# Optimization experiments

Measured on AMD Instinct MI355X. Metric: run time of the kernel, lower is better.

## Reference

```python
import jax, jax.numpy as jnp
import numpy as np

EPS = 1e-5

def layer_norm(x, g, b):
    mu = jnp.mean(x, axis=-1, keepdims=True)
    var = jnp.mean(jnp.square(x - mu), axis=-1, keepdims=True)
    return (x - mu) * jax.lax.rsqrt(var + EPS) * g + b

def setup_inputs() -> dict:
    B, T, C, H = 8, 1024, 1024, 16
    hs = C // H
    key = jax.random.key(0)
    ks = jax.random.split(key, 12)
    s = 0.02
    return {
        "x": jax.random.normal(ks[0], (B, T, C), dtype=jnp.float32),
        # per-head projections, stacked: [H, C, hs]
        "wq": jax.random.normal(ks[1], (H, C, hs), dtype=jnp.float32) * s,
        "wk": jax.random.normal(ks[2], (H, C, hs), dtype=jnp.float32) * s,
        "wv": jax.random.normal(ks[3], (H, C, hs), dtype=jnp.float32) * s,
        "w_proj": jax.random.normal(ks[4], (C, C), dtype=jnp.float32) * s,
        "b_proj": jnp.zeros((C,), dtype=jnp.float32),
        "ln1_g": jnp.ones((C,), dtype=jnp.float32),
        "ln1_b": jnp.zeros((C,), dtype=jnp.float32),
        "ln2_g": jnp.ones((C,), dtype=jnp.float32),
        "ln2_b": jnp.zeros((C,), dtype=jnp.float32),
        "w1": jax.random.normal(ks[5], (C, 4 * C), dtype=jnp.float32) * s,
        "b1": jnp.zeros((4 * C,), dtype=jnp.float32),
        "w2": jax.random.normal(ks[6], (4 * C, C), dtype=jnp.float32) * s,
        "b2": jnp.zeros((C,), dtype=jnp.float32),
    }

def reference(x, wq, wk, wv, w_proj, b_proj, ln1_g, ln1_b, ln2_g, ln2_b, w1, b1, w2, b2):
    B, T, C = x.shape
    # --- self-attention (pre-norm) ---
    h = layer_norm(x, ln1_g, ln1_b)                      # [B,T,C]
    q = jnp.einsum('btc,hcd->bhtd', h, wq)               # [B,H,T,hs]
    k = jnp.einsum('btc,hcd->bhtd', h, wk)
    v = jnp.einsum('btc,hcd->bhtd', h, wv)
    # NOTE: original scales by C**-0.5 with C = n_embed (not head_size)
    scores = jnp.einsum('bhtd,bhsd->bhts', q, k) * (C ** -0.5)
    causal = jnp.tril(jnp.ones((T, T), dtype=bool))
    scores = jnp.where(causal, scores, -jnp.inf)
    att = jax.nn.softmax(scores, axis=-1)                # dropout is identity (eval)
    out = jnp.einsum('bhts,bhsd->bhtd', att, v)          # [B,H,T,hs]
    out = out.transpose(0, 2, 1, 3).reshape(B, T, C)     # concat heads
    x = x + out @ w_proj + b_proj
    # --- feed-forward (pre-norm) ---
    h2 = layer_norm(x, ln2_g, ln2_b)
    x = x + jax.nn.relu(h2 @ w1 + b1) @ w2 + b2
    return x
```

## Files before the change

kernel.cpp:

```cpp
#include <hip/hip_runtime.h>
#include <cstdint>

typedef __attribute__((ext_vector_type(8))) __bf16 bf16x8;
typedef __attribute__((ext_vector_type(4))) float f32x4;

__device__ __forceinline__ unsigned short f2bf(float f) {
  union { float f; unsigned int u; } v; v.f = f;
  unsigned int u = v.u;
  return (unsigned short)((u + 0x7FFFu + ((u >> 16) & 1u)) >> 16);
}

__device__ __forceinline__ void load_lds16(const unsigned short* g, unsigned short* l) {
  __builtin_amdgcn_global_load_lds(
      (const __attribute__((address_space(1))) unsigned int*)g,
      (__attribute__((address_space(3))) unsigned int*)l, 16, 0, 0);
}

__global__ void prep_kernel(const float* __restrict__ wq, const float* __restrict__ wk,
                            const float* __restrict__ wv, const float* __restrict__ w_proj,
                            const float* __restrict__ w1, const float* __restrict__ w2,
                            const float* __restrict__ x, const float* __restrict__ ln1_g,
                            const float* __restrict__ ln1_b,
                            unsigned short* __restrict__ qkvt, unsigned short* __restrict__ projt,
                            unsigned short* __restrict__ w1t, unsigned short* __restrict__ w2t,
                            unsigned short* __restrict__ h1) {
  __shared__ float tile[32][33];
  __shared__ float a1[4], a2[4];
  const int id = blockIdx.x;
  const int tid = threadIdx.x;

  if (id >= 12288) {
    const int row = id - 12288;
    const int wave = tid >> 6, lane = tid & 63;
    const float4 xv = *(const float4*)&x[(long)row * 1024 + tid * 4];
    float s1 = xv.x + xv.y + xv.z + xv.w;
    float s2 = xv.x * xv.x + xv.y * xv.y + xv.z * xv.z + xv.w * xv.w;
#pragma unroll
    for (int m = 1; m < 64; m <<= 1) { s1 += __shfl_xor(s1, m); s2 += __shfl_xor(s2, m); }
    if (lane == 0) { a1[wave] = s1; a2[wave] = s2; }
    __syncthreads();
    s1 = a1[0] + a1[1] + a1[2] + a1[3];
    s2 = a2[0] + a2[1] + a2[2] + a2[3];
    const float mu = s1 * (1.f / 1024.f);
    const float var = s2 * (1.f / 1024.f) - mu * mu;
    const float rs = rsqrtf(var + 1e-5f);
    const float4 gv = *(const float4*)&ln1_g[tid * 4];
    const float4 bv = *(const float4*)&ln1_b[tid * 4];
    ushort4 o;
    o.x = f2bf((xv.x - mu) * rs * gv.x + bv.x);
    o.y = f2bf((xv.y - mu) * rs * gv.y + bv.y);
    o.z = f2bf((xv.z - mu) * rs * gv.z + bv.z);
    o.w = f2bf((xv.w - mu) * rs * gv.w + bv.w);
    *(ushort4*)&h1[(long)row * 1024 + tid * 4] = o;
    return;
  }

  const float* src;
  unsigned short* dst;
  int K, N, nt, kt;
  if (id < 3072) {
    const int which = id >> 10, rem = id & 1023;
    const int slice = rem >> 6, t = rem & 63;
    src = (which == 0 ? wq : which == 1 ? wk : wv) + (long)slice * 65536;
    dst = qkvt + (long)which * 1048576 + (long)slice * 65536;
    K = 1024; N = 64;
    nt = (t & 1) * 32; kt = (t >> 1) * 32;
  } else if (id < 4096) {
    const int t = id - 3072;
    src = w_proj; dst = projt; K = 1024; N = 1024;
    nt = (t & 31) * 32; kt = (t >> 5) * 32;
  } else if (id < 8192) {
    const int t = id - 4096;
    src = w1; dst = w1t; K = 1024; N = 4096;
    nt = (t & 127) * 32; kt = (t >> 7) * 32;
  } else {
    const int t = id - 8192;
    src = w2; dst = w2t; K = 4096; N = 1024;
    nt = (t & 31) * 32; kt = (t >> 5) * 32;
  }
  const int tx = tid & 31, ty = tid >> 5;
#pragma unroll
  for (int i = 0; i < 4; i++)
    tile[ty + 8 * i][tx] = src[(long)(kt + ty + 8 * i) * N + nt + tx];
  __syncthreads();
#pragma unroll
  for (int i = 0; i < 4; i++)
    dst[(long)(nt + ty + 8 * i) * K + kt + tx] = f2bf(tile[tx][ty + 8 * i]);
}

__global__ __launch_bounds__(256, 4) void ln_kernel(const float* __restrict__ x,
                                                    const float* __restrict__ g,
                                                    const float* __restrict__ b,
                                                    unsigned short* __restrict__ out) {
  const int row = blockIdx.x, tid = threadIdx.x;
  const int wave = tid >> 6, lane = tid & 63;
  const float4 xv = *(const float4*)&x[(long)row * 1024 + tid * 4];
  float s1 = xv.x + xv.y + xv.z + xv.w;
  float s2 = xv.x * xv.x + xv.y * xv.y + xv.z * xv.z + xv.w * xv.w;
#pragma unroll
  for (int m = 1; m < 64; m <<= 1) { s1 += __shfl_xor(s1, m); s2 += __shfl_xor(s2, m); }
  __shared__ float a1[4], a2[4];
  if (lane == 0) { a1[wave] = s1; a2[wave] = s2; }
  __syncthreads();
  s1 = a1[0] + a1[1] + a1[2] + a1[3];
  s2 = a2[0] + a2[1] + a2[2] + a2[3];
  const float mu = s1 * (1.f / 1024.f);
  const float var = s2 * (1.f / 1024.f) - mu * mu;
  const float rs = rsqrtf(var + 1e-5f);
  const float4 gv = *(const float4*)&g[tid * 4];
  const float4 bv = *(const float4*)&b[tid * 4];
  ushort4 o;
  o.x = f2bf((xv.x - mu) * rs * gv.x + bv.x);
  o.y = f2bf((xv.y - mu) * rs * gv.y + bv.y);
  o.z = f2bf((xv.z - mu) * rs * gv.z + bv.z);
  o.w = f2bf((xv.w - mu) * rs * gv.w + bv.w);
  *(ushort4*)&out[(long)row * 1024 + tid * 4] = o;
}

#define EPI_QKV 0
#define EPI_F32 1
#define EPI_RELU 2

template <int EPI>
__global__ __launch_bounds__(256, 3) void gemm_bt(
    const unsigned short* __restrict__ A, const unsigned short* __restrict__ Bt,
    int M, int N, int K,
    const float* __restrict__ bias, const float* __restrict__ resid,
    float* __restrict__ outF, unsigned short* __restrict__ outB,
    unsigned short* __restrict__ qb, unsigned short* __restrict__ kb,
    unsigned short* __restrict__ vTb) {
  __shared__ __attribute__((aligned(16))) unsigned short Alds[128 * 64];
  __shared__ __attribute__((aligned(16))) unsigned short Blds[128 * 64];
  const int tid = threadIdx.x;
  const int wave = tid >> 6, lane = tid & 63;
  const int quad = lane >> 4, l15 = lane & 15;
  const long tM = (long)blockIdx.x * 128;
  const long tN = (long)blockIdx.y * 128;
  const int wm = (wave >> 1) * 64, wn = (wave & 1) * 64;

  const unsigned short* aP[4];
  const unsigned short* bP[4];
  unsigned short* lA[4];
  unsigned short* lB[4];
#pragma unroll
  for (int qq = 0; qq < 4; qq++) {
    int p = (qq * 4 + wave) * 64 + lane;
    int m = p >> 3;
    int kc = (p & 7) ^ (m & 7);
    aP[qq] = A + (tM + m) * K + kc * 8;
    bP[qq] = Bt + (tN + m) * K + kc * 8;
    lA[qq] = Alds + (qq * 4 + wave) * 512;
    lB[qq] = Blds + (qq * 4 + wave) * 512;
  }

  f32x4 acc[4][4];
#pragma unroll
  for (int i = 0; i < 4; i++)
#pragma unroll
    for (int j = 0; j < 4; j++) acc[i][j] = (f32x4){0.f, 0.f, 0.f, 0.f};

  for (int k0 = 0; k0 < K; k0 += 64) {
    __syncthreads();
#pragma unroll
    for (int qq = 0; qq < 4; qq++) {
      load_lds16(aP[qq], lA[qq]);
      load_lds16(bP[qq], lB[qq]);
      aP[qq] += 64;
      bP[qq] += 64;
    }
    __syncthreads();
#pragma unroll
    for (int ks = 0; ks < 2; ks++) {
      bf16x8 af[4], bfr[4];
#pragma unroll
      for (int mt = 0; mt < 4; mt++) {
        int ml = wm + mt * 16 + l15;
        int pc = (ks * 4 + quad) ^ (ml & 7);
        af[mt] = *(const bf16x8*)&Alds[(ml * 8 + pc) * 8];
      }
#pragma unroll
      for (int nt = 0; nt < 4; nt++) {
        int nl = wn + nt * 16 + l15;
        int pc = (ks * 4 + quad) ^ (nl & 7);
        bfr[nt] = *(const bf16x8*)&Blds[(nl * 8 + pc) * 8];
      }
#pragma unroll
      for (int mt = 0; mt < 4; mt++)
#pragma unroll
        for (int nt = 0; nt < 4; nt++)
          acc[mt][nt] = __builtin_amdgcn_mfma_f32_16x16x32_bf16(af[mt], bfr[nt], acc[mt][nt], 0, 0, 0);
    }
  }

#pragma unroll
  for (int mt = 0; mt < 4; mt++) {
#pragma unroll
    for (int nt = 0; nt < 4; nt++) {
      const long col = tN + wn + nt * 16 + l15;
      const long row0 = tM + wm + mt * 16 + quad * 4;
      if (EPI == EPI_F32) {
        const float bv = bias[col];
#pragma unroll
        for (int r = 0; r < 4; r++) {
          long idx = (row0 + r) * N + col;
          outF[idx] = acc[mt][nt][r] + bv + resid[idx];
        }
      } else if (EPI == EPI_RELU) {
        const float bv = bias[col];
#pragma unroll
        for (int r = 0; r < 4; r++) {
          float v = acc[mt][nt][r] + bv;
          outB[(row0 + r) * N + col] = f2bf(v > 0.f ? v : 0.f);
        }
      } else {
        const int which = (int)(col >> 10);
        const int hh = (int)((col >> 6) & 15);
        const int dd = (int)(col & 63);
        const int b = (int)(row0 >> 10), t0 = (int)(row0 & 1023);
        if (which == 2) {
          ushort4 pk;
          pk.x = f2bf(acc[mt][nt][0]);
          pk.y = f2bf(acc[mt][nt][1]);
          pk.z = f2bf(acc[mt][nt][2]);
          pk.w = f2bf(acc[mt][nt][3]);
          *(ushort4*)&vTb[(long)(b * 16 + hh) * 65536 + dd * 1024 + t0] = pk;
        } else {
          unsigned short* dst = (which == 0 ? qb : kb);
#pragma unroll
          for (int r = 0; r < 4; r++)
            dst[((b * 16 + hh) * 1024 + t0 + r) * 64 + dd] = f2bf(acc[mt][nt][r]);
        }
      }
    }
  }
}

__global__ __launch_bounds__(256, 2) void attn_kernel(const unsigned short* __restrict__ qb,
                                                      const unsigned short* __restrict__ kb,
                                                      const unsigned short* __restrict__ vTb,
                                                      unsigned short* __restrict__ out) {
  __shared__ __attribute__((aligned(16))) unsigned short Klds[2][64 * 64];
  __shared__ __attribute__((aligned(16))) unsigned short Vlds[2][64 * 64];
  __shared__ __attribute__((aligned(16))) unsigned short Plds[4 * 16 * 68];
  const int bh = blockIdx.x;
  const int j = blockIdx.y;
  const int tid = threadIdx.x;
  const int wave = tid >> 6, lane = tid & 63;
  const int quad = lane >> 4, l15 = lane & 15;

  const unsigned short* qp = qb + (long)bh * 65536;
  const unsigned short* kp = kb + (long)bh * 65536;
  const unsigned short* vp = vTb + (long)bh * 65536;
  const int b = bh >> 4, h = bh & 15;

  unsigned short* Pl = Plds + wave * (16 * 68);
  const float cscale = 0.045084220f;

  for (int ph = 0; ph < 2; ph++) {
    const int qt2 = ph ? 7 - j : j;

    bf16x8 qf[2][2];
#pragma unroll
    for (int g = 0; g < 2; g++) {
      const int qrow = qt2 * 128 + (wave * 2 + g) * 16 + l15;
      qf[g][0] = *(const bf16x8*)&qp[qrow * 64 + quad * 8];
      qf[g][1] = *(const bf16x8*)&qp[qrow * 64 + 32 + quad * 8];
    }

    f32x4 O[2][4];
    float l_r[2][4];
#pragma unroll
    for (int g = 0; g < 2; g++) {
#pragma unroll
      for (int nt = 0; nt < 4; nt++) O[g][nt] = (f32x4){0.f, 0.f, 0.f, 0.f};
#pragma unroll
      for (int r = 0; r < 4; r++) l_r[g][r] = 0.f;
    }

    const int nstage = qt2 + 1;
    for (int st = 0; st < nstage; st++) {
      __syncthreads();
#pragma unroll
      for (int c = 0; c < 4; c++) {
        const int pb = c * 256 + wave * 64;
        const int p = pb + lane;
        const int sub = p >> 9;
        const int q_ = p & 511;
        const int m = q_ >> 3;
        const int kc = (q_ & 7) ^ (m & 7);
        const int kt = st * 2 + sub;
        load_lds16(kp + (kt * 64 + m) * 64 + kc * 8, (unsigned short*)Klds + pb * 8);
        load_lds16(vp + m * 1024 + kt * 64 + kc * 8, (unsigned short*)Vlds + pb * 8);
      }
      __syncthreads();

#pragma unroll
      for (int sub = 0; sub < 2; sub++) {
        const int kt = st * 2 + sub;
        const unsigned short* Ksub = (const unsigned short*)Klds + sub * 4096;
        const unsigned short* Vsub = (const unsigned short*)Vlds + sub * 4096;

#pragma unroll
        for (int g = 0; g < 2; g++) {
          const int rowbase = qt2 * 128 + (wave * 2 + g) * 16;
          if (kt * 64 >= rowbase + 16) continue;

          f32x4 S[4];
#pragma unroll
          for (int nt = 0; nt < 4; nt++) {
            const int row = nt * 16 + l15;
            const int pc0 = quad ^ (row & 7);
            const int pc1 = (quad + 4) ^ (row & 7);
            bf16x8 kf0 = *(const bf16x8*)&Ksub[(row * 8 + pc0) * 8];
            bf16x8 kf1 = *(const bf16x8*)&Ksub[(row * 8 + pc1) * 8];
            f32x4 s = (f32x4){0.f, 0.f, 0.f, 0.f};
            s = __builtin_amdgcn_mfma_f32_16x16x32_bf16(qf[g][0], kf0, s, 0, 0, 0);
            s = __builtin_amdgcn_mfma_f32_16x16x32_bf16(qf[g][1], kf1, s, 0, 0, 0);
            S[nt] = s;
          }

          const bool diag = (kt * 64 + 63 > rowbase);
          const int tb = rowbase + quad * 4;
#pragma unroll
          for (int nt = 0; nt < 4; nt++) {
            const int sg = kt * 64 + nt * 16 + l15;
#pragma unroll
            for (int r = 0; r < 4; r++) {
              float pv = exp2f(S[nt][r] * cscale);
              if (diag && sg > tb + r) pv = 0.f;
              l_r[g][r] += pv;
              Pl[(quad * 4 + r) * 68 + nt * 16 + l15] = f2bf(pv);
            }
          }
          __threadfence_block();

#pragma unroll
          for (int ks2 = 0; ks2 < 2; ks2++) {
            bf16x8 pa = *(const bf16x8*)&Pl[l15 * 68 + ks2 * 32 + quad * 8];
#pragma unroll
            for (int nt = 0; nt < 4; nt++) {
              const int d = nt * 16 + l15;
              const int pc = (ks2 * 4 + quad) ^ (d & 7);
              bf16x8 vf = *(const bf16x8*)&Vsub[(d * 8 + pc) * 8];
              O[g][nt] = __builtin_amdgcn_mfma_f32_16x16x32_bf16(pa, vf, O[g][nt], 0, 0, 0);
            }
          }
          __threadfence_block();
        }
      }
    }

#pragma unroll
    for (int g = 0; g < 2; g++) {
#pragma unroll
      for (int r = 0; r < 4; r++) {
        float lv = l_r[g][r];
        lv += __shfl_xor(lv, 1);
        lv += __shfl_xor(lv, 2);
        lv += __shfl_xor(lv, 4);
        lv += __shfl_xor(lv, 8);
        lv = __builtin_amdgcn_rcpf(lv);
        const int t = qt2 * 128 + (wave * 2 + g) * 16 + quad * 4 + r;
#pragma unroll
        for (int nt = 0; nt < 4; nt++)
          out[(long)(b * 1024 + t) * 1024 + h * 64 + nt * 16 + l15] = f2bf(O[g][nt][r] * lv);
      }
    }
  }
}

extern "C" void kernel_launch(void* const* d_in, const int* in_sizes, int n_in,
                              void* d_out, int out_size, void* d_ws, size_t ws_size,
                              hipStream_t stream) {
  const float* x = (const float*)d_in[0];
  const float* wq = (const float*)d_in[1];
  const float* wk = (const float*)d_in[2];
  const float* wv = (const float*)d_in[3];
  const float* w_proj = (const float*)d_in[4];
  const float* b_proj = (const float*)d_in[5];
  const float* ln1_g = (const float*)d_in[6];
  const float* ln1_b = (const float*)d_in[7];
  const float* ln2_g = (const float*)d_in[8];
  const float* ln2_b = (const float*)d_in[9];
  const float* w1 = (const float*)d_in[10];
  const float* b1 = (const float*)d_in[11];
  const float* w2 = (const float*)d_in[12];
  const float* b2 = (const float*)d_in[13];
  float* out = (float*)d_out;

  char* w = (char*)d_ws;
  unsigned short* h1 = (unsigned short*)w;      w += (size_t)8192 * 1024 * 2;
  unsigned short* wqkvt = (unsigned short*)w;   w += (size_t)3072 * 1024 * 2;
  unsigned short* wprojt = (unsigned short*)w;  w += (size_t)1024 * 1024 * 2;
  unsigned short* w1t = (unsigned short*)w;     w += (size_t)4096 * 1024 * 2;
  unsigned short* w2t = (unsigned short*)w;     w += (size_t)4096 * 1024 * 2;
  unsigned short* qbuf = (unsigned short*)w;    w += (size_t)128 * 1024 * 64 * 2;
  unsigned short* kbuf = (unsigned short*)w;    w += (size_t)128 * 1024 * 64 * 2;
  unsigned short* vTbuf = (unsigned short*)w;   w += (size_t)128 * 1024 * 64 * 2;
  unsigned short* act = (unsigned short*)w;     w += (size_t)8192 * 4096 * 2;
  unsigned short* attnO = h1;
  unsigned short* h2 = qbuf;

  prep_kernel<<<12288 + 8192, 256, 0, stream>>>(wq, wk, wv, w_proj, w1, w2,
                                                x, ln1_g, ln1_b,
                                                wqkvt, wprojt, w1t, w2t, h1);

  gemm_bt<EPI_QKV><<<dim3(64, 24), 256, 0, stream>>>(h1, wqkvt, 8192, 3072, 1024,
                                                     nullptr, nullptr, nullptr, nullptr,
                                                     qbuf, kbuf, vTbuf);

  attn_kernel<<<dim3(128, 4), 256, 0, stream>>>(qbuf, kbuf, vTbuf, attnO);

  gemm_bt<EPI_F32><<<dim3(64, 8), 256, 0, stream>>>(attnO, wprojt, 8192, 1024, 1024,
                                                    b_proj, x, out, nullptr,
                                                    nullptr, nullptr, nullptr);

  ln_kernel<<<8192, 256, 0, stream>>>(out, ln2_g, ln2_b, h2);

  gemm_bt<EPI_RELU><<<dim3(64, 32), 256, 0, stream>>>(h2, w1t, 8192, 4096, 1024,
                                                      b1, nullptr, nullptr, act,
                                                      nullptr, nullptr, nullptr);

  gemm_bt<EPI_F32><<<dim3(64, 8), 256, 0, stream>>>(act, w2t, 8192, 1024, 4096,
                                                    b2, out, out, nullptr,
                                                    nullptr, nullptr, nullptr);
}
```

Measured before the change: 438.4 us.

## Move proj/FFN weight transposes into the QKV GEMM launch as extra blocks

Splits the prep kernel so it only converts the QKV weights and runs layernorm 1. The projection and FFN weight transpose-to-bf16 work is appended as trailing blocks of a dedicated QKV GEMM kernel. The aim is to overlap the memory-bound weight conversion with the compute-bound QKV GEMM and shorten the critical path of the prep stage. In exchange, the GEMM kernel carries extra shared memory for the transpose tile and has heterogeneous blocks, which could affect occupancy or scheduling.

Result: no change. 440.2 us (+0.4%).

```diff
diff --git a/kernel.cpp b/kernel.cpp
--- a/kernel.cpp
+++ b/kernel.cpp
@@ -16,21 +16,18 @@
       (__attribute__((address_space(3))) unsigned int*)l, 16, 0, 0);
 }
 
-__global__ void prep_kernel(const float* __restrict__ wq, const float* __restrict__ wk,
-                            const float* __restrict__ wv, const float* __restrict__ w_proj,
-                            const float* __restrict__ w1, const float* __restrict__ w2,
-                            const float* __restrict__ x, const float* __restrict__ ln1_g,
-                            const float* __restrict__ ln1_b,
-                            unsigned short* __restrict__ qkvt, unsigned short* __restrict__ projt,
-                            unsigned short* __restrict__ w1t, unsigned short* __restrict__ w2t,
-                            unsigned short* __restrict__ h1) {
+__global__ void prep1_kernel(const float* __restrict__ wq, const float* __restrict__ wk,
+                             const float* __restrict__ wv,
+                             const float* __restrict__ x, const float* __restrict__ ln1_g,
+                             const float* __restrict__ ln1_b,
+                             unsigned short* __restrict__ qkvt, unsigned short* __restrict__ h1) {
   __shared__ float tile[32][33];
   __shared__ float a1[4], a2[4];
   const int id = blockIdx.x;
   const int tid = threadIdx.x;
 
-  if (id >= 12288) {
-    const int row = id - 12288;
+  if (id >= 3072) {
+    const int row = id - 3072;
     const int wave = tid >> 6, lane = tid & 63;
     const float4 xv = *(const float4*)&x[(long)row * 1024 + tid * 4];
     float s1 = xv.x + xv.y + xv.z + xv.w;
@@ -55,37 +52,19 @@
     return;
   }
 
-  const float* src;
-  unsigned short* dst;
-  int K, N, nt, kt;
-  if (id < 3072) {
-    const int which = id >> 10, rem = id & 1023;
-    const int slice = rem >> 6, t = rem & 63;
-    src = (which == 0 ? wq : which == 1 ? wk : wv) + (long)slice * 65536;
-    dst = qkvt + (long)which * 1048576 + (long)slice * 65536;
-    K = 1024; N = 64;
-    nt = (t & 1) * 32; kt = (t >> 1) * 32;
-  } else if (id < 4096) {
-    const int t = id - 3072;
-    src = w_proj; dst = projt; K = 1024; N = 1024;
-    nt = (t & 31) * 32; kt = (t >> 5) * 32;
-  } else if (id < 8192) {
-    const int t = id - 4096;
-    src = w1; dst = w1t; K = 1024; N = 4096;
-    nt = (t & 127) * 32; kt = (t >> 7) * 32;
-  } else {
-    const int t = id - 8192;
-    src = w2; dst = w2t; K = 4096; N = 1024;
-    nt = (t & 31) * 32; kt = (t >> 5) * 32;
-  }
+  const int which = id >> 10, rem = id & 1023;
+  const int slice = rem >> 6, t = rem & 63;
+  const float* src = (which == 0 ? wq : which == 1 ? wk : wv) + (long)slice * 65536;
+  unsigned short* dst = qkvt + (long)which * 1048576 + (long)slice * 65536;
+  const int nt = (t & 1) * 32, kt = (t >> 1) * 32;
   const int tx = tid & 31, ty = tid >> 5;
 #pragma unroll
   for (int i = 0; i < 4; i++)
-    tile[ty + 8 * i][tx] = src[(long)(kt + ty + 8 * i) * N + nt + tx];
+    tile[ty + 8 * i][tx] = src[(long)(kt + ty + 8 * i) * 64 + nt + tx];
   __syncthreads();
 #pragma unroll
   for (int i = 0; i < 4; i++)
-    dst[(long)(nt + ty + 8 * i) * K + kt + tx] = f2bf(tile[tx][ty + 8 * i]);
+    dst[(long)(nt + ty + 8 * i) * 1024 + kt + tx] = f2bf(tile[tx][ty + 8 * i]);
 }
 
 __global__ __launch_bounds__(256, 4) void ln_kernel(const float* __restrict__ x,
@@ -117,7 +96,6 @@
   *(ushort4*)&out[(long)row * 1024 + tid * 4] = o;
 }
 
-#define EPI_QKV 0
 #define EPI_F32 1
 #define EPI_RELU 2
 
@@ -126,9 +104,7 @@
     const unsigned short* __restrict__ A, const unsigned short* __restrict__ Bt,
     int M, int N, int K,
     const float* __restrict__ bias, const float* __restrict__ resid,
-    float* __restrict__ outF, unsigned short* __restrict__ outB,
-    unsigned short* __restrict__ qb, unsigned short* __restrict__ kb,
-    unsigned short* __restrict__ vTb) {
+    float* __restrict__ outF, unsigned short* __restrict__ outB) {
   __shared__ __attribute__((aligned(16))) unsigned short Alds[128 * 64];
   __shared__ __attribute__((aligned(16))) unsigned short Blds[128 * 64];
   const int tid = threadIdx.x;
@@ -198,38 +174,149 @@
     for (int nt = 0; nt < 4; nt++) {
       const long col = tN + wn + nt * 16 + l15;
       const long row0 = tM + wm + mt * 16 + quad * 4;
+      const float bv = bias[col];
       if (EPI == EPI_F32) {
-        const float bv = bias[col];
 #pragma unroll
         for (int r = 0; r < 4; r++) {
           long idx = (row0 + r) * N + col;
           outF[idx] = acc[mt][nt][r] + bv + resid[idx];
         }
-      } else if (EPI == EPI_RELU) {
-        const float bv = bias[col];
+      } else {
 #pragma unroll
         for (int r = 0; r < 4; r++) {
           float v = acc[mt][nt][r] + bv;
           outB[(row0 + r) * N + col] = f2bf(v > 0.f ? v : 0.f);
         }
+      }
+    }
+  }
+}
+
+__global__ __launch_bounds__(256, 3) void gemm_qkv(
+    const unsigned short* __restrict__ A, const unsigned short* __restrict__ Bt,
+    unsigned short* __restrict__ qb, unsigned short* __restrict__ kb,
+    unsigned short* __restrict__ vTb,
+    const float* __restrict__ w_proj, const float* __restrict__ w1,
+    const float* __restrict__ w2,
+    unsigned short* __restrict__ projt, unsigned short* __restrict__ w1t,
+    unsigned short* __restrict__ w2t) {
+  __shared__ __attribute__((aligned(16))) unsigned short Alds[128 * 64];
+  __shared__ __attribute__((aligned(16))) unsigned short Blds[128 * 64];
+  __shared__ float tile[32][33];
+  const int tid = threadIdx.x;
+  const int bx = blockIdx.x;
+
+  if (bx >= 1536) {
+    const int id = bx - 1536;
+    const float* src;
+    unsigned short* dst;
+    int K, N, nt, kt;
+    if (id < 1024) {
+      src = w_proj; dst = projt; K = 1024; N = 1024;
+      nt = (id & 31) * 32; kt = (id >> 5) * 32;
+    } else if (id < 5120) {
+      const int t = id - 1024;
+      src = w1; dst = w1t; K = 1024; N = 4096;
+      nt = (t & 127) * 32; kt = (t >> 7) * 32;
+    } else {
+      const int t = id - 5120;
+      src = w2; dst = w2t; K = 4096; N = 1024;
+      nt = (t & 31) * 32; kt = (t >> 5) * 32;
+    }
+    const int tx = tid & 31, ty = tid >> 5;
+#pragma unroll
+    for (int i = 0; i < 4; i++)
+      tile[ty + 8 * i][tx] = src[(long)(kt + ty + 8 * i) * N + nt + tx];
+    __syncthreads();
+#pragma unroll
+    for (int i = 0; i < 4; i++)
+      dst[(long)(nt + ty + 8 * i) * K + kt + tx] = f2bf(tile[tx][ty + 8 * i]);
+    return;
+  }
+
+  const int wave = tid >> 6, lane = tid & 63;
+  const int quad = lane >> 4, l15 = lane & 15;
+  const long tM = (long)(bx & 63) * 128;
+  const long tN = (long)(bx >> 6) * 128;
+  const int wm = (wave >> 1) * 64, wn = (wave & 1) * 64;
+  const int K = 1024;
+
+  const unsigned short* aP[4];
+  const unsigned short* bP[4];
+  unsigned short* lA[4];
+  unsigned short* lB[4];
+#pragma unroll
+  for (int qq = 0; qq < 4; qq++) {
+    int p = (qq * 4 + wave) * 64 + lane;
+    int m = p >> 3;
+    int kc = (p & 7) ^ (m & 7);
+    aP[qq] = A + (tM + m) * K + kc * 8;
+    bP[qq] = Bt + (tN + m) * K + kc * 8;
+    lA[qq] = Alds + (qq * 4 + wave) * 512;
+    lB[qq] = Blds + (qq * 4 + wave) * 512;
+  }
+
+  f32x4 acc[4][4];
+#pragma unroll
+  for (int i = 0; i < 4; i++)
+#pragma unroll
+    for (int j = 0; j < 4; j++) acc[i][j] = (f32x4){0.f, 0.f, 0.f, 0.f};
+
+  for (int k0 = 0; k0 < K; k0 += 64) {
+    __syncthreads();
+#pragma unroll
+    for (int qq = 0; qq < 4; qq++) {
+      load_lds16(aP[qq], lA[qq]);
+      load_lds16(bP[qq], lB[qq]);
+      aP[qq] += 64;
+      bP[qq] += 64;
+    }
+    __syncthreads();
+#pragma unroll
+    for (int ks = 0; ks < 2; ks++) {
+      bf16x8 af[4], bfr[4];
+#pragma unroll
+      for (int mt = 0; mt < 4; mt++) {
+        int ml = wm + mt * 16 + l15;
+        int pc = (ks * 4 + quad) ^ (ml & 7);
+        af[mt] = *(const bf16x8*)&Alds[(ml * 8 + pc) * 8];
+      }
+#pragma unroll
+      for (int nt = 0; nt < 4; nt++) {
+        int nl = wn + nt * 16 + l15;
+        int pc = (ks * 4 + quad) ^ (nl & 7);
+        bfr[nt] = *(const bf16x8*)&Blds[(nl * 8 + pc) * 8];
+      }
+#pragma unroll
+      for (int mt = 0; mt < 4; mt++)
+#pragma unroll
+        for (int nt = 0; nt < 4; nt++)
+          acc[mt][nt] = __builtin_amdgcn_mfma_f32_16x16x32_bf16(af[mt], bfr[nt], acc[mt][nt], 0, 0, 0);
+    }
+  }
+
+#pragma unroll
+  for (int mt = 0; mt < 4; mt++) {
+#pragma unroll
+    for (int nt = 0; nt < 4; nt++) {
+      const long col = tN + wn + nt * 16 + l15;
+      const long row0 = tM + wm + mt * 16 + quad * 4;
+      const int which = (int)(col >> 10);
+      const int hh = (int)((col >> 6) & 15);
+      const int dd = (int)(col & 63);
+      const int b = (int)(row0 >> 10), t0 = (int)(row0 & 1023);
+      if (which == 2) {
+        ushort4 pk;
+        pk.x = f2bf(acc[mt][nt][0]);
+        pk.y = f2bf(acc[mt][nt][1]);
+        pk.z = f2bf(acc[mt][nt][2]);
+        pk.w = f2bf(acc[mt][nt][3]);
+        *(ushort4*)&vTb[(long)(b * 16 + hh) * 65536 + dd * 1024 + t0] = pk;
       } else {
-        const int which = (int)(col >> 10);
-        const int hh = (int)((col >> 6) & 15);
-        const int dd = (int)(col & 63);
-        const int b = (int)(row0 >> 10), t0 = (int)(row0 & 1023);
-        if (which == 2) {
-          ushort4 pk;
-          pk.x = f2bf(acc[mt][nt][0]);
-          pk.y = f2bf(acc[mt][nt][1]);
-          pk.z = f2bf(acc[mt][nt][2]);
-          pk.w = f2bf(acc[mt][nt][3]);
-          *(ushort4*)&vTb[(long)(b * 16 + hh) * 65536 + dd * 1024 + t0] = pk;
-        } else {
-          unsigned short* dst = (which == 0 ? qb : kb);
-#pragma unroll
-          for (int r = 0; r < 4; r++)
-            dst[((b * 16 + hh) * 1024 + t0 + r) * 64 + dd] = f2bf(acc[mt][nt][r]);
-        }
+        unsigned short* dst = (which == 0 ? qb : kb);
+#pragma unroll
+        for (int r = 0; r < 4; r++)
+          dst[((b * 16 + hh) * 1024 + t0 + r) * 64 + dd] = f2bf(acc[mt][nt][r]);
       }
     }
   }
@@ -401,27 +488,21 @@
   unsigned short* attnO = h1;
   unsigned short* h2 = qbuf;
 
-  prep_kernel<<<12288 + 8192, 256, 0, stream>>>(wq, wk, wv, w_proj, w1, w2,
-                                                x, ln1_g, ln1_b,
-                                                wqkvt, wprojt, w1t, w2t, h1);
-
-  gemm_bt<EPI_QKV><<<dim3(64, 24), 256, 0, stream>>>(h1, wqkvt, 8192, 3072, 1024,
-                                                     nullptr, nullptr, nullptr, nullptr,
-                                                     qbuf, kbuf, vTbuf);
+  prep1_kernel<<<3072 + 8192, 256, 0, stream>>>(wq, wk, wv, x, ln1_g, ln1_b, wqkvt, h1);
+
+  gemm_qkv<<<1536 + 9216, 256, 0, stream>>>(h1, wqkvt, qbuf, kbuf, vTbuf,
+                                            w_proj, w1, w2, wprojt, w1t, w2t);
 
   attn_kernel<<<dim3(128, 4), 256, 0, stream>>>(qbuf, kbuf, vTbuf, attnO);
 
   gemm_bt<EPI_F32><<<dim3(64, 8), 256, 0, stream>>>(attnO, wprojt, 8192, 1024, 1024,
-                                                    b_proj, x, out, nullptr,
-                                                    nullptr, nullptr, nullptr);
+                                                    b_proj, x, out, nullptr);
 
   ln_kernel<<<8192, 256, 0, stream>>>(out, ln2_g, ln2_b, h2);
 
   gemm_bt<EPI_RELU><<<dim3(64, 32), 256, 0, stream>>>(h2, w1t, 8192, 4096, 1024,
-                                                      b1, nullptr, nullptr, act,
-                                                      nullptr, nullptr, nullptr);
+                                                      b1, nullptr, nullptr, act);
 
   gemm_bt<EPI_F32><<<dim3(64, 8), 256, 0, stream>>>(act, w2t, 8192, 1024, 4096,
-                                                    b2, out, out, nullptr,
-                                                    nullptr, nullptr, nullptr);
-}
+                                                    b2, out, out, nullptr);
+}
```
